# Kernel optimization log

Hardware: AMD Instinct MI355X
Metric: run time of the kernel (lower is better)

## Reference

```python
import jax, jax.numpy as jnp
import numpy as np

L, D, H, FFN, V = 24, 512, 16, 2048, 1025
HD = D // H
TOP_K = 15
REP_PEN = 1.35


def _layernorm(x, w, b, eps=1e-5):
    m = jnp.mean(x, -1, keepdims=True)
    var = jnp.var(x, -1, keepdims=True)
    return (x - m) / jnp.sqrt(var + eps) * w + b


def _sine_pe(T, d):
    pos = jnp.arange(T, dtype=jnp.float32)[:, None]
    div = jnp.exp(jnp.arange(0, d, 2, dtype=jnp.float32) * (-np.log(10000.0) / d))
    pe = jnp.zeros((T, d), jnp.float32)
    pe = pe.at[:, 0::2].set(jnp.sin(pos * div))
    pe = pe.at[:, 1::2].set(jnp.cos(pos * div))
    return pe


def setup_inputs():
    S, Ty, B = 2047, 1535, 1
    key = jax.random.key(0)
    ks = jax.random.split(key, 16)
    n = lambda i, sh, s=0.02: jax.random.normal(ks[i], sh, jnp.float32) * s
    return {
        "y": jax.random.randint(ks[0], (B, Ty + 1), 0, V, jnp.int32),
        "k": n(1, (L, S, B, D), 1.0),
        "v": n(2, (L, S, B, D), 1.0),
        "y_emb": n(3, (B, Ty, D), 1.0),
        "x_example": n(4, (B, 512), 1.0),
        "alpha": jnp.ones((1,), jnp.float32),
        "emb_table": n(5, (V, D)),
        "in_proj_w": n(6, (L, 3 * D, D)),
        "in_proj_b": jnp.zeros((L, 3 * D), jnp.float32),
        "out_w": n(7, (L, D, D)),
        "out_b": jnp.zeros((L, D), jnp.float32),
        "ln1_w": jnp.ones((L, D), jnp.float32),
        "ln1_b": jnp.zeros((L, D), jnp.float32),
        "ln2_w": jnp.ones((L, D), jnp.float32),
        "ln2_b": jnp.zeros((L, D), jnp.float32),
        "ffn_w1": n(8, (L, FFN, D)),
        "ffn_b1": jnp.zeros((L, FFN), jnp.float32),
        "ffn_w2": n(9, (L, D, FFN)),
        "ffn_b2": jnp.zeros((L, D), jnp.float32),
        "pred_w": n(10, (V, D)),
        "pred_b": jnp.zeros((V,), jnp.float32),
        "noise": jax.random.normal(ks[11], (V,), jnp.float32),
    }


def reference(y, k, v, y_emb, x_example, alpha, emb_table,
              in_proj_w, in_proj_b, out_w, out_b,
              ln1_w, ln1_b, ln2_w, ln2_b,
              ffn_w1, ffn_b1, ffn_w2, ffn_b2,
              pred_w, pred_b, noise):
    B = y.shape[0]
    # pad KV caches by one slot along seq dim (dim 1) -> [L, S+1, B, D]
    k_pad = jnp.pad(k, ((0, 0), (0, 1), (0, 0), (0, 0)))
    v_pad = jnp.pad(v, ((0, 0), (0, 1), (0, 0), (0, 0)))

    # embed newest token, extend y_emb cache
    new_emb = emb_table[y[:, -1:]]                       # [B,1,D]
    y_emb_new = jnp.concatenate([y_emb, new_emb], axis=1)  # [B,T,D]
    T = y_emb_new.shape[1]
    pe = _sine_pe(T, D)
    y_pos = y_emb_new + alpha * pe[None]                 # scale=False -> x_scale=1
    x = y_pos[:, -1:]                                    # [B,1,D] single query token

    scale = 1.0 / jnp.sqrt(jnp.float32(HD))

    def scan_body(x, per):
        kl, vl, wqkv, bqkv, wo, bo, g1, b1, g2, b2, fw1, fb1, fw2, fb2 = per
        qkv = jnp.einsum('bqd,ed->bqe', x, wqkv) + bqkv  # [B,1,3D]
        q, k_new, v_new = jnp.split(qkv, 3, axis=-1)
        kl = kl.at[-1].set(k_new[:, 0])                  # write into last cache slot
        vl = vl.at[-1].set(v_new[:, 0])
        qh = q.reshape(B, 1, H, HD)
        kh = kl.reshape(-1, B, H, HD)                    # [S+1,B,H,hd]
        vh = vl.reshape(-1, B, H, HD)
        scores = jnp.einsum('bqhd,sbhd->bhqs', qh, kh) * scale
        attn = jax.nn.softmax(scores, axis=-1)
        ctx = jnp.einsum('bhqs,sbhd->bqhd', attn, vh).reshape(B, 1, D)
        attn_out = jnp.einsum('bqd,ed->bqe', ctx, wo) + bo
        x = _layernorm(x + attn_out, g1, b1)             # post-LN (torch default)
        hdn = jax.nn.relu(jnp.einsum('bqd,fd->bqf', x, fw1) + fb1)
        ff = jnp.einsum('bqf,df->bqd', hdn, fw2) + fb2
        x = _layernorm(x + ff, g2, b2)
        return x, (kl, vl)

    x, (k_out, v_out) = jax.lax.scan(
        scan_body, x,
        (k_pad, v_pad, in_proj_w, in_proj_b, out_w, out_b,
         ln1_w, ln1_b, ln2_w, ln2_b, ffn_w1, ffn_b1, ffn_w2, ffn_b2))

    logits = jnp.einsum('bd,vd->bv', x[:, -1], pred_w) + pred_b  # [B,V]

    # ---- sampling on logits[0] ----
    lg = logits[0]
    prev = y[0]
    # repetition penalty (gather -> transform -> scatter; dup indices write same value)
    score = lg[prev]
    score = jnp.where(score < 0, score * REP_PEN, score / REP_PEN)
    lg = lg.at[prev].set(score)
    # top_p == 1.0 -> skipped; temperature == 1.0
    pivot = jax.lax.top_k(lg, TOP_K)[0][-1]
    lg = jnp.where(lg < pivot, -jnp.inf, lg)
    probs = jax.nn.softmax(lg)
    # faithful to source: argmax(probs / randn_like(probs))
    samples = jnp.argmax(probs / noise).astype(jnp.int32)[None, None]  # [1,1]
    y_new = jnp.concatenate([y, samples.astype(y.dtype)], axis=1)
    return y_new, k_out, v_out, y_emb_new, logits, samples
```

## Files before the change

### kernel.cpp

```cpp
#include <hip/hip_runtime.h>
#include <math.h>

#define LL 24
#define DD 512
#define HH 16
#define FFD 2048
#define VV 1025
#define SS 2047
#define TKV 2048
#define TYY 1535
#define NBLK 256
#define NT 512

typedef float f4v __attribute__((ext_vector_type(4)));

constexpr size_t O_YNEW  = 0;
constexpr size_t O_KOUT  = 1537;
constexpr size_t O_VOUT  = O_KOUT + (size_t)LL*TKV*DD;
constexpr size_t O_YEMB  = O_VOUT + (size_t)LL*TKV*DD;
constexpr size_t O_LOGITS= O_YEMB + (size_t)(TYY+1)*DD;
constexpr size_t O_SAMP  = O_LOGITS + VV;

constexpr int W_FFA  = 0;
constexpr int W_WY   = 8192;
constexpr int W_PART = 16384;
constexpr int W_KN   = 25088;
constexpr int W_VN   = 25600;

struct P {
  const int* y; const float* k; const float* v; const float* yemb;
  const float* alpha; const float* emb;
  const float* ipw; const float* ipb; const float* ow; const float* ob;
  const float* l1w; const float* l1b; const float* l2w; const float* l2b;
  const float* f1w; const float* f1b; const float* f2w; const float* f2b;
  const float* pw; const float* pb; const float* noise;
  float* out; float* ws;
};

__device__ __forceinline__ float dot4(float4 a, float4 b){
  return a.x*b.x + a.y*b.y + a.z*b.z + a.w*b.w;
}
__device__ __forceinline__ float ldv(const float* pp){
  return __hip_atomic_load(pp, __ATOMIC_RELAXED, __HIP_MEMORY_SCOPE_AGENT);
}
__device__ __forceinline__ void stv(float* pp, float v){
  __hip_atomic_store(pp, v, __ATOMIC_RELAXED, __HIP_MEMORY_SCOPE_AGENT);
}
__device__ __forceinline__ unsigned ldu(const unsigned* pp){
  return __hip_atomic_load(pp, __ATOMIC_RELAXED, __HIP_MEMORY_SCOPE_AGENT);
}

__device__ __forceinline__ void lbar(){
  asm volatile("s_waitcnt lgkmcnt(0)" ::: "memory");
  __builtin_amdgcn_s_barrier();
  __builtin_amdgcn_sched_barrier(0);
}
__device__ __forceinline__ void barr_arrive(unsigned* flags, unsigned ph){
  asm volatile("s_waitcnt vmcnt(0) lgkmcnt(0)" ::: "memory");
  __builtin_amdgcn_s_barrier();
  __builtin_amdgcn_sched_barrier(0);
  if (threadIdx.x == 0)
    __hip_atomic_store(&flags[blockIdx.x*16], ph, __ATOMIC_RELAXED, __HIP_MEMORY_SCOPE_AGENT);
}
__device__ __forceinline__ void barr_wait(unsigned* flags, unsigned ph){
  const int t = threadIdx.x;
  if (t < 64){
    for (;;){
      int ok = 1;
      #pragma unroll
      for (int i=0;i<4;++i) ok &= (int)(ldu(&flags[(t*4+i)*16]) >= ph);
      if (__all(ok)) break;
    }
  }
  __builtin_amdgcn_s_barrier();
  asm volatile("" ::: "memory");
}
__device__ __forceinline__ void barr_wait_head(unsigned* flags, unsigned ph, int h){
  const int t = threadIdx.x;
  if (t < 64){
    for (;;){
      int ok = 1;
      if (t < 16) ok = (int)(ldu(&flags[(t*16 + h)*16]) >= ph);
      if (__all(ok)) break;
    }
  }
  __builtin_amdgcn_s_barrier();
  asm volatile("" ::: "memory");
}

__device__ __forceinline__ float2 bsum2(float a, float b2, float2* r8, int t){
  for (int off=32; off; off>>=1){ a += __shfl_xor(a, off); b2 += __shfl_xor(b2, off); }
  lbar();
  if ((t & 63) == 0) r8[t >> 6] = make_float2(a, b2);
  lbar();
  float2 s = r8[0];
  #pragma unroll
  for (int i=1;i<8;++i){ s.x += r8[i].x; s.y += r8[i].y; }
  return s;
}
__device__ __forceinline__ void ln512g(float r, float g, float bb,
                                       float* dst, float2* r8, int t)
{
  float2 s = bsum2(r, r*r, r8, t);
  float mean = s.x * (1.f/512.f);
  float var  = fmaxf(s.y * (1.f/512.f) - mean*mean, 0.f);
  dst[t] = (r - mean) * rsqrtf(var + 1e-5f) * g + bb;
}
__device__ __forceinline__ void bargmax(float v, int i, float* r8v, int* r8i,
                                        int t, float& ov, int& oi)
{
  for (int off=32; off; off>>=1){
    float v2 = __shfl_xor(v, off); int i2 = __shfl_xor(i, off);
    if (v2 > v || (v2 == v && i2 < i)){ v = v2; i = i2; }
  }
  lbar();
  if ((t & 63) == 0){ r8v[t>>6] = v; r8i[t>>6] = i; }
  lbar();
  ov = r8v[0]; oi = r8i[0];
  #pragma unroll
  for (int kk=1; kk<8; ++kk){
    float v2 = r8v[kk]; int i2 = r8i[kk];
    if (v2 > ov || (v2 == ov && i2 < oi)){ ov = v2; oi = i2; }
  }
}

struct RegsQ  { float4 w[8]; float b[4]; };
struct RegsKV { float4 k0,k1,v0,v1; };
struct RegsTl { float4 t0,t1; float bias; };
struct RegsLN { float g2,b2,fb2; };
struct RegsBC { float2 oww; float4 f1p0,f1p1,f2p0,f2p1;
                float g1,b1,obv,f1bv; };

__device__ __forceinline__ void issueQ(const P& p, int l, int h, int t, RegsQ& q){
  const int lane = t & 63, w = t >> 6;
  const float* Wb = p.ipw + (size_t)l*1536*DD;
  const float* Bb = p.ipb + (size_t)l*1536;
  #pragma unroll
  for (int pp=0; pp<4; ++pp){
    int row = h*32 + w + 8*pp;
    const float4* wr = (const float4*)(Wb + (size_t)row*DD);
    q.w[2*pp] = wr[lane]; q.w[2*pp+1] = wr[lane+64];
    q.b[pp] = Bb[row];
  }
}
__device__ __forceinline__ void issueL(const P& p, int b, int t, RegsQ& q){
  const int lane = t & 63, w = t >> 6;
  int row = (w < 4) ? b*4 + w : ((b == 255 && w == 4) ? 1024 : -1);
  if (row >= 0){
    const float4* wr = (const float4*)(p.pw + (size_t)row*DD);
    q.w[0] = wr[lane]; q.w[1] = wr[lane+64];
    q.b[0] = p.pb[row];
  }
}
__device__ __forceinline__ void issueKV(const P& p, int l, int h, int c, int t,
                                        RegsKV& kv){
  const float* kb = p.k + (size_t)l*SS*DD;
  const float* vb = p.v + (size_t)l*SS*DD;
  const int s0 = c*128;
  kv.k0 = kv.v0 = kv.k1 = kv.v1 = make_float4(0,0,0,0);
  {
    int row = t >> 3, c4 = (t & 7)*4, s = s0 + row;
    if (s < SS){
      kv.k0 = *(const float4*)&kb[(size_t)s*DD + h*32 + c4];
      kv.v0 = *(const float4*)&vb[(size_t)s*DD + h*32 + c4];
    }
  }
  {
    int idx = t + NT;
    int row = idx >> 3, c4 = (idx & 7)*4, s = s0 + row;
    if (s < SS){
      kv.k1 = *(const float4*)&kb[(size_t)s*DD + h*32 + c4];
      kv.v1 = *(const float4*)&vb[(size_t)s*DD + h*32 + c4];
    }
  }
}
__device__ __forceinline__ void issueTl(const P& p, int l, int h, int c, int t,
                                        RegsTl& tl){
  const int lane = t & 63, w = t >> 6;
  if (w < 4){
    int isv = w >> 1;
    int row = 512 + isv*512 + h*32 + c*2 + (w&1);
    const float4* wr = (const float4*)(p.ipw + (size_t)l*1536*DD + (size_t)row*DD);
    tl.t0 = wr[lane]; tl.t1 = wr[lane+64];
    tl.bias = p.ipb[(size_t)l*1536 + row];
  }
}
__device__ __forceinline__ void issueLN(const P& p, int l, int t, RegsLN& r){
  r.g2 = p.l2w[(size_t)l*DD + t];
  r.b2 = p.l2b[(size_t)l*DD + t];
  r.fb2= p.f2b[(size_t)l*DD + t];
}
__device__ __forceinline__ void issueBCsmall(const P& p, int l, int b, int h,
                                             int c, int t, RegsBC& bc){
  bc.oww = *(const float2*)(p.ow + (size_t)l*DD*DD
            + (size_t)(c*32 + (t>>4))*DD + h*32 + (t&15)*2);
  bc.f1bv = p.f1b[(size_t)l*FFD + b*8 + (t>>6)];
  bc.g1  = p.l1w[(size_t)l*DD + t];
  bc.b1  = p.l1b[(size_t)l*DD + t];
  bc.obv = p.ob[(size_t)l*DD + t];
}
__device__ __forceinline__ void issueBCw(const P& p, int l, int b, int t,
                                         RegsBC& bc){
  const int lane = t & 63, w = t >> 6;
  {
    int f = b*8 + w;
    const float4* wr = (const float4*)(p.f1w + (size_t)l*FFD*DD + (size_t)f*DD);
    bc.f1p0 = wr[lane]; bc.f1p1 = wr[lane+64];
  }
  {
    const float* wr = p.f2w + (size_t)l*DD*FFD + (size_t)t*FFD + b*8;
    bc.f2p0 = *(const float4*)wr;
    bc.f2p1 = *(const float4*)(wr+4);
  }
}

__global__ __launch_bounds__(NT, 1) void mega_kernel(P p)
{
  __shared__ __align__(16) float S_kl[128*33];
  __shared__ __align__(16) float S_vl[128*33];
  __shared__ __align__(16) float S_x[512];
  __shared__ float S_ps[128];
  __shared__ float S_cacc[512];
  __shared__ float S_pb[544];
  __shared__ float S_q[32];
  __shared__ float S_kn[32];
  __shared__ float S_vn[32];
  __shared__ float S_ctx[32];
  __shared__ float S_scal[4];
  __shared__ float S_hdn[8];
  __shared__ float2 S_r82[8];
  __shared__ float S_r8v[8];
  __shared__ int   S_r8i[8];

  const int t = threadIdx.x, b = blockIdx.x;
  const int lane = t & 63, w = t >> 6;
  const int h = b & 15, c = b >> 4;
  unsigned* flags = (unsigned*)p.ws;
  float* wsd = p.ws + 4352;
  float* out = p.out;
  unsigned ph = 0;

  RegsQ q; RegsKV kv; RegsTl tl; RegsLN lnp; RegsBC bc;
  issueQ(p, 0, h, t, q);
  issueKV(p, 0, h, c, t, kv);
  issueTl(p, 0, h, c, t, tl);
  issueBCw(p, 0, b, t, bc);

  for (int l = 0; l < LL; ++l){
    float fs = 0.f;
    if (l > 0){
      const float* fb = wsd + W_FFA + (size_t)((l+1)&1)*4096;
      #pragma unroll
      for (int i=0;i<8;++i) fs += ldv(&fb[i*512 + t]);
    }
    issueBCsmall(p, l, b, h, c, t, bc);

    if (l == 0){
      int tok = p.y[1535];
      float a0 = p.alpha[0];
      float ev = p.emb[(size_t)tok*DD + t];
      float ang = 1535.0f * expf((float)(2*(t>>1)) * (-9.210340371976184f/512.0f));
      float pe = (t & 1) ? cosf(ang) : sinf(ang);
      S_x[t] = ev + a0*pe;
      if (b == 0) for (int i=t;i<1536;i+=NT)
        __builtin_nontemporal_store((float)p.y[i], out + O_YNEW + i);
      if (b == 1)
        __builtin_nontemporal_store(ev, out + O_YEMB + (size_t)TYY*DD + t);
      lbar();
    } else {
      float r = S_x[t] + lnp.fb2 + fs;
      ln512g(r, lnp.g2, lnp.b2, S_x, S_r82, t);
      lbar();
    }

    #pragma unroll
    for (int pp=0; pp<4; ++pp){
      float s = dot4(q.w[2*pp],   ((const float4*)S_x)[lane])
              + dot4(q.w[2*pp+1], ((const float4*)S_x)[lane+64]);
      for (int off=32; off; off>>=1) s += __shfl_xor(s, off);
      if (lane == 0) S_q[w + 8*pp] = s + q.b[pp];
    }
    if (w < 4){
      int isv = w >> 1;
      int col = h*32 + c*2 + (w & 1);
      float s = dot4(tl.t0, ((const float4*)S_x)[lane])
              + dot4(tl.t1, ((const float4*)S_x)[lane+64]);
      for (int off=32; off; off>>=1) s += __shfl_xor(s, off);
      if (lane == 0){
        float val = s + tl.bias;
        stv(&wsd[(isv ? W_VN : W_KN) + col], val);
        __builtin_nontemporal_store(val,
          out + (isv ? O_VOUT : O_KOUT) + (size_t)l*TKV*DD + (size_t)SS*DD + col);
      }
    }
    {
      int r0 = t >> 3, c40 = (t & 7)*4;
      int lb = r0*33 + c40;
      S_kl[lb+0]=kv.k0.x; S_kl[lb+1]=kv.k0.y; S_kl[lb+2]=kv.k0.z; S_kl[lb+3]=kv.k0.w;
      S_vl[lb+0]=kv.v0.x; S_vl[lb+1]=kv.v0.y; S_vl[lb+2]=kv.v0.z; S_vl[lb+3]=kv.v0.w;
      int idx = t + NT;
      int r1 = idx >> 3, c41 = (idx & 7)*4;
      int lb1 = r1*33 + c41;
      S_kl[lb1+0]=kv.k1.x; S_kl[lb1+1]=kv.k1.y; S_kl[lb1+2]=kv.k1.z; S_kl[lb1+3]=kv.k1.w;
      S_vl[lb1+0]=kv.v1.x; S_vl[lb1+1]=kv.v1.y; S_vl[lb1+2]=kv.v1.z; S_vl[lb1+3]=kv.v1.w;
    }
    lbar();

    {
      const int s0 = c*128;
      float pv = 0.f;
      if (t < 128 && (s0 + t) < SS){
        float acc = 0.f;
        #pragma unroll
        for (int j=0;j<32;++j) acc += S_kl[t*33+j]*S_q[j];
        pv = expf(acc * 0.17677669529663687f);
      }
      if (t < 128) S_ps[t] = pv;
      lbar();
      int g = t >> 5, j = t & 31;
      float ca = 0.f;
      #pragma unroll
      for (int i=0;i<8;++i){ int r = g*8+i; ca += S_ps[r]*S_vl[r*33+j]; }
      S_cacc[g*32 + j] = ca;
      lbar();
      float* pbase = wsd + W_PART + (size_t)(h*16+c)*34;
      if (t < 32){
        float v2 = 0.f;
        #pragma unroll
        for (int gg=0; gg<16; ++gg) v2 += S_cacc[gg*32 + t];
        stv(&pbase[t], v2);
      } else if (t >= 64 && t < 128){
        int ll2 = t - 64;
        float dv = S_ps[ll2] + S_ps[ll2+64];
        for (int off=32; off; off>>=1) dv += __shfl_xor(dv, off);
        if (ll2 == 0) stv(&pbase[32], dv);
      }
    }
    barr_arrive(flags, ++ph);
    {
      const int s0 = c*128;
      float* ko = out + O_KOUT + (size_t)l*TKV*DD;
      float* vo = out + O_VOUT + (size_t)l*TKV*DD;
      {
        int row = t >> 3, c4 = (t & 7)*4, s = s0 + row;
        if (s < SS){
          size_t go = (size_t)s*DD + h*32 + c4;
          __builtin_nontemporal_store(kv.k0.x, ko+go);
          __builtin_nontemporal_store(kv.k0.y, ko+go+1);
          __builtin_nontemporal_store(kv.k0.z, ko+go+2);
          __builtin_nontemporal_store(kv.k0.w, ko+go+3);
          __builtin_nontemporal_store(kv.v0.x, vo+go);
          __builtin_nontemporal_store(kv.v0.y, vo+go+1);
          __builtin_nontemporal_store(kv.v0.z, vo+go+2);
          __builtin_nontemporal_store(kv.v0.w, vo+go+3);
        }
      }
      {
        int idx = t + NT;
        int row = idx >> 3, c4 = (idx & 7)*4, s = s0 + row;
        if (s < SS){
          size_t go = (size_t)s*DD + h*32 + c4;
          __builtin_nontemporal_store(kv.k1.x, ko+go);
          __builtin_nontemporal_store(kv.k1.y, ko+go+1);
          __builtin_nontemporal_store(kv.k1.z, ko+go+2);
          __builtin_nontemporal_store(kv.k1.w, ko+go+3);
          __builtin_nontemporal_store(kv.v1.x, vo+go);
          __builtin_nontemporal_store(kv.v1.y, vo+go+1);
          __builtin_nontemporal_store(kv.v1.z, vo+go+2);
          __builtin_nontemporal_store(kv.v1.w, vo+go+3);
        }
      }
    }
    barr_wait_head(flags, ph, h);

    {
      for (int i=t; i<544; i+=NT) S_pb[i] = ldv(&wsd[W_PART + h*544 + i]);
      if (t < 32){ S_kn[t] = ldv(&wsd[W_KN + h*32 + t]); S_vn[t] = ldv(&wsd[W_VN + h*32 + t]); }
      lbar();
      if (t < 32){
        float tsp = S_q[t] * S_kn[t];
        for (int off=16; off; off>>=1) tsp += __shfl_xor(tsp, off, 32);
        if (t == 0){
          float et = expf(tsp * 0.17677669529663687f);
          float den = et;
          #pragma unroll
          for (int cc=0; cc<16; ++cc) den += S_pb[cc*34+32];
          S_scal[0] = et; S_scal[1] = den;
        }
      }
      lbar();
      if (t < 32){
        float cv = S_scal[0] * S_vn[t];
        #pragma unroll
        for (int cc=0; cc<16; ++cc) cv += S_pb[cc*34 + t];
        S_ctx[t] = cv / S_scal[1];
      }
      lbar();
      int j2 = (t & 15) * 2;
      float s = bc.oww.x*S_ctx[j2] + bc.oww.y*S_ctx[j2+1];
      s += __shfl_xor(s, 8, 16); s += __shfl_xor(s, 4, 16);
      s += __shfl_xor(s, 2, 16); s += __shfl_xor(s, 1, 16);
      if ((t & 15) == 0) stv(&wsd[W_WY + h*512 + c*32 + (t>>4)], s);
    }
    barr_arrive(flags, ++ph);
    if (l < 23){
      issueKV(p, l+1, h, c, t, kv);
      issueTl(p, l+1, h, c, t, tl);
    }
    issueLN(p, l, t, lnp);
    barr_wait(flags, ph);

    {
      float xs = 0.f;
      #pragma unroll
      for (int i=0;i<16;++i) xs += ldv(&wsd[W_WY + i*512 + t]);
      float r = S_x[t] + bc.obv + xs;
      ln512g(r, bc.g1, bc.b1, S_x, S_r82, t);
      lbar();
      {
        float s = dot4(bc.f1p0, ((const float4*)S_x)[lane])
                + dot4(bc.f1p1, ((const float4*)S_x)[lane+64]);
        for (int off=32; off; off>>=1) s += __shfl_xor(s, off);
        if (lane == 0) S_hdn[w] = fmaxf(s + bc.f1bv, 0.f);
      }
      lbar();
      float con = bc.f2p0.x*S_hdn[0]+bc.f2p0.y*S_hdn[1]
                + bc.f2p0.z*S_hdn[2]+bc.f2p0.w*S_hdn[3]
                + bc.f2p1.x*S_hdn[4]+bc.f2p1.y*S_hdn[5]
                + bc.f2p1.z*S_hdn[6]+bc.f2p1.w*S_hdn[7];
      atomicAdd(&wsd[W_FFA + (size_t)(l&1)*4096 + (size_t)(b&7)*512 + t], con);
      if (t < 16) stv(&wsd[W_FFA + (size_t)((l+1)&1)*4096 + b*16 + t], 0.f);
    }
    barr_arrive(flags, ++ph);
    if (l < 23){
      issueQ(p, l+1, h, t, q);
      issueBCw(p, l+1, b, t, bc);
    } else {
      issueL(p, b, t, q);
    }
    barr_wait(flags, ph);
  }

  {
    float fs = 0.f;
    const float* fb = wsd + W_FFA + (size_t)((LL-1)&1)*4096;
    #pragma unroll
    for (int i=0;i<8;++i) fs += ldv(&fb[i*512 + t]);
    float r = S_x[t] + lnp.fb2 + fs;
    ln512g(r, lnp.g2, lnp.b2, S_x, S_r82, t);
    lbar();
    if (w < 4 || (b == 255 && w == 4)){
      int row = (w < 4) ? b*4 + w : 1024;
      float s = dot4(q.w[0], ((const float4*)S_x)[lane])
              + dot4(q.w[1], ((const float4*)S_x)[lane+64]);
      for (int off=32; off; off>>=1) s += __shfl_xor(s, off);
      if (lane == 0) stv(&out[O_LOGITS+row], s + q.b[0]);
    }
  }
  barr_arrive(flags, ++ph);
  barr_wait(flags, ph);

  if (b == 0){
    float* lg  = S_kl;
    float* lgc = S_kl + 1025;
    int*   pen = (int*)(S_kl + 2050);
    for (int i=t;i<VV;i+=NT){ lg[i] = ldv(&out[O_LOGITS+i]); pen[i]=0; }
    lbar();
    for (int i=t;i<1536;i+=NT) pen[p.y[i]] = 1;
    lbar();
    for (int i=t;i<VV;i+=NT){
      if (pen[i]){ float s = lg[i]; lg[i] = (s<0.f) ? s*1.35f : s/1.35f; }
    }
    lbar();
    for (int i=t;i<VV;i+=NT) lgc[i]=lg[i];
    lbar();
    float sM = 0.f, sPiv = 0.f;
    for (int it=0; it<15; ++it){
      float bv = -INFINITY; int bi = VV;
      for (int i=t;i<VV;i+=NT){ float v2=lgc[i]; if (v2>bv){bv=v2;bi=i;} }
      float ov; int oi;
      bargmax(bv, bi, S_r8v, S_r8i, t, ov, oi);
      if (it==0)  sM   = ov;
      if (it==14) sPiv = ov;
      if (t==0) lgc[oi] = -INFINITY;
      lbar();
    }
    float zl = 0.f;
    for (int i=t;i<VV;i+=NT){
      float lv = lg[i];
      float pv2 = (lv < sPiv) ? 0.f : expf(lv - sM);
      lgc[i] = pv2; zl += pv2;
    }
    {
      float2 s = bsum2(zl, 0.f, S_r82, t);
      zl = s.x;
    }
    lbar();
    float bv=-INFINITY; int bi=VV;
    for (int i=t;i<VV;i+=NT){
      float val = (lgc[i]/zl)/p.noise[i];
      if (val>bv){bv=val;bi=i;}
    }
    float ov; int oi;
    bargmax(bv, bi, S_r8v, S_r8i, t, ov, oi);
    if (t==0){
      float sf = (float)oi;
      out[O_SAMP] = sf;
      out[O_YNEW+1536] = sf;
    }
  } else {
    const int nf4 = (TYY*DD - 4)/4;
    for (int qq = (b-1)*NT + t; qq < nf4; qq += 255*NT){
      float4 a = *(const float4*)&p.yemb[qq*4];
      float4 bq = *(const float4*)&p.yemb[qq*4 + 4];
      f4v o = {a.w, bq.x, bq.y, bq.z};
      __builtin_nontemporal_store(o, (f4v*)(out + O_YEMB + 3 + (size_t)qq*4));
    }
    if (b == 1){
      if (t < 3) __builtin_nontemporal_store(p.yemb[t], out + O_YEMB + t);
      if (t == 3) __builtin_nontemporal_store(p.yemb[TYY*DD-1], out + O_YEMB + TYY*DD - 1);
    }
  }
}

extern "C" void kernel_launch(void* const* d_in, const int* in_sizes, int n_in,
                              void* d_out, int out_size, void* d_ws, size_t ws_size,
                              hipStream_t stream)
{
  P p;
  p.y    = (const int*)d_in[0];
  p.k    = (const float*)d_in[1];
  p.v    = (const float*)d_in[2];
  p.yemb = (const float*)d_in[3];
  p.alpha= (const float*)d_in[5];
  p.emb  = (const float*)d_in[6];
  p.ipw  = (const float*)d_in[7];
  p.ipb  = (const float*)d_in[8];
  p.ow   = (const float*)d_in[9];
  p.ob   = (const float*)d_in[10];
  p.l1w  = (const float*)d_in[11];
  p.l1b  = (const float*)d_in[12];
  p.l2w  = (const float*)d_in[13];
  p.l2b  = (const float*)d_in[14];
  p.f1w  = (const float*)d_in[15];
  p.f1b  = (const float*)d_in[16];
  p.f2w  = (const float*)d_in[17];
  p.f2b  = (const float*)d_in[18];
  p.pw   = (const float*)d_in[19];
  p.pb   = (const float*)d_in[20];
  p.noise= (const float*)d_in[21];
  p.out  = (float*)d_out;
  p.ws   = (float*)d_ws;

  hipMemsetAsync(d_ws, 0, 50176, stream);
  void* args[] = { &p };
  hipLaunchCooperativeKernel((void*)mega_kernel, dim3(NBLK), dim3(NT), args, 0, stream);
}
```

Baseline: 470.7 us.

## Remove per-head barrier by atomically accumulating unnormalized attention output projections

Each block now multiplies its unnormalized partial attention numerator directly by its slice of the output projection and atomically adds the result into a double-buffered workspace. Softmax denominators are also atomically summed per head and applied as reciprocals when the residual is formed. This removes the per-head grid barrier phase and its partial-result gather. The chunk-15 block now computes the full new K/V rows for its head in place of the distributed per-block rows. The exchange is more atomic traffic, more registers for the larger Q/K/V weight prefetch, a larger workspace memset, and the new-token logit is no longer softmax-stabilized (it enters via exp through the shared path).

```diff
diff --git a/kernel.cpp b/kernel.cpp
--- a/kernel.cpp
+++ b/kernel.cpp
@@ -21,11 +21,9 @@
 constexpr size_t O_LOGITS= O_YEMB + (size_t)(TYY+1)*DD;
 constexpr size_t O_SAMP  = O_LOGITS + VV;
 
-constexpr int W_FFA  = 0;
-constexpr int W_WY   = 8192;
-constexpr int W_PART = 16384;
-constexpr int W_KN   = 25088;
-constexpr int W_VN   = 25600;
+constexpr int W_WYA = 0;
+constexpr int W_DEN = 16384;
+constexpr int W_FFA = 16896;
 
 struct P {
   const int* y; const float* k; const float* v; const float* yemb;
@@ -75,18 +73,6 @@
   __builtin_amdgcn_s_barrier();
   asm volatile("" ::: "memory");
 }
-__device__ __forceinline__ void barr_wait_head(unsigned* flags, unsigned ph, int h){
-  const int t = threadIdx.x;
-  if (t < 64){
-    for (;;){
-      int ok = 1;
-      if (t < 16) ok = (int)(ldu(&flags[(t*16 + h)*16]) >= ph);
-      if (__all(ok)) break;
-    }
-  }
-  __builtin_amdgcn_s_barrier();
-  asm volatile("" ::: "memory");
-}
 
 __device__ __forceinline__ float2 bsum2(float a, float b2, float2* r8, int t){
   for (int off=32; off; off>>=1){ a += __shfl_xor(a, off); b2 += __shfl_xor(b2, off); }
@@ -124,14 +110,14 @@
   }
 }
 
-struct RegsQ  { float4 w[8]; float b[4]; };
+struct RegsQX { float4 w[24]; float b[12]; };
 struct RegsKV { float4 k0,k1,v0,v1; };
-struct RegsTl { float4 t0,t1; float bias; };
 struct RegsLN { float g2,b2,fb2; };
-struct RegsBC { float2 oww; float4 f1p0,f1p1,f2p0,f2p1;
-                float g1,b1,obv,f1bv; };
-
-__device__ __forceinline__ void issueQ(const P& p, int l, int h, int t, RegsQ& q){
+struct RegsW  { float4 w[8]; };
+struct RegsBC { float4 f1p0,f1p1,f2p0,f2p1; float g1,b1,obv,f1bv; };
+
+__device__ __forceinline__ void issueQX(const P& p, int l, int h, int c, int t,
+                                        RegsQX& q){
   const int lane = t & 63, w = t >> 6;
   const float* Wb = p.ipw + (size_t)l*1536*DD;
   const float* Bb = p.ipb + (size_t)l*1536;
@@ -142,8 +128,18 @@
     q.w[2*pp] = wr[lane]; q.w[2*pp+1] = wr[lane+64];
     q.b[pp] = Bb[row];
   }
-}
-__device__ __forceinline__ void issueL(const P& p, int b, int t, RegsQ& q){
+  if (c == 15){
+    #pragma unroll
+    for (int pp=4; pp<12; ++pp){
+      int r = w + 8*((pp-4)&3);
+      int row = ((pp < 8) ? 512 : 1024) + h*32 + r;
+      const float4* wr = (const float4*)(Wb + (size_t)row*DD);
+      q.w[2*pp] = wr[lane]; q.w[2*pp+1] = wr[lane+64];
+      q.b[pp] = Bb[row];
+    }
+  }
+}
+__device__ __forceinline__ void issueL(const P& p, int b, int t, RegsQX& q){
   const int lane = t & 63, w = t >> 6;
   int row = (w < 4) ? b*4 + w : ((b == 255 && w == 4) ? 1024 : -1);
   if (row >= 0){
@@ -174,32 +170,24 @@
     }
   }
 }
-__device__ __forceinline__ void issueTl(const P& p, int l, int h, int c, int t,
-                                        RegsTl& tl){
-  const int lane = t & 63, w = t >> 6;
-  if (w < 4){
-    int isv = w >> 1;
-    int row = 512 + isv*512 + h*32 + c*2 + (w&1);
-    const float4* wr = (const float4*)(p.ipw + (size_t)l*1536*DD + (size_t)row*DD);
-    tl.t0 = wr[lane]; tl.t1 = wr[lane+64];
-    tl.bias = p.ipb[(size_t)l*1536 + row];
-  }
-}
 __device__ __forceinline__ void issueLN(const P& p, int l, int t, RegsLN& r){
   r.g2 = p.l2w[(size_t)l*DD + t];
   r.b2 = p.l2b[(size_t)l*DD + t];
   r.fb2= p.f2b[(size_t)l*DD + t];
 }
-__device__ __forceinline__ void issueBCsmall(const P& p, int l, int b, int h,
-                                             int c, int t, RegsBC& bc){
-  bc.oww = *(const float2*)(p.ow + (size_t)l*DD*DD
-            + (size_t)(c*32 + (t>>4))*DD + h*32 + (t&15)*2);
+__device__ __forceinline__ void issueW(const P& p, int l, int h, int t, RegsW& wsl){
+  const float4* wr = (const float4*)(p.ow + (size_t)l*DD*DD + (size_t)t*DD + h*32);
+  #pragma unroll
+  for (int i=0;i<8;++i) wsl.w[i] = wr[i];
+}
+__device__ __forceinline__ void issueBCsmall(const P& p, int l, int b, int t,
+                                             RegsBC& bc){
   bc.f1bv = p.f1b[(size_t)l*FFD + b*8 + (t>>6)];
   bc.g1  = p.l1w[(size_t)l*DD + t];
   bc.b1  = p.l1b[(size_t)l*DD + t];
   bc.obv = p.ob[(size_t)l*DD + t];
 }
-__device__ __forceinline__ void issueBCw(const P& p, int l, int b, int t,
+__device__ __forceinline__ void issueF12(const P& p, int l, int b, int t,
                                          RegsBC& bc){
   const int lane = t & 63, w = t >> 6;
   {
@@ -221,11 +209,9 @@
   __shared__ __align__(16) float S_x[512];
   __shared__ float S_ps[128];
   __shared__ float S_cacc[512];
-  __shared__ float S_pb[544];
   __shared__ float S_q[32];
-  __shared__ float S_kn[32];
-  __shared__ float S_vn[32];
-  __shared__ float S_ctx[32];
+  __shared__ __align__(16) float S_num[32];
+  __shared__ float S_rcp[16];
   __shared__ float S_scal[4];
   __shared__ float S_hdn[8];
   __shared__ float2 S_r82[8];
@@ -240,20 +226,20 @@
   float* out = p.out;
   unsigned ph = 0;
 
-  RegsQ q; RegsKV kv; RegsTl tl; RegsLN lnp; RegsBC bc;
-  issueQ(p, 0, h, t, q);
+  RegsQX qx; RegsKV kv; RegsLN lnp; RegsW wsl; RegsBC bc;
+  issueQX(p, 0, h, c, t, qx);
   issueKV(p, 0, h, c, t, kv);
-  issueTl(p, 0, h, c, t, tl);
-  issueBCw(p, 0, b, t, bc);
 
   for (int l = 0; l < LL; ++l){
+    const int par = l & 1, np = (l+1) & 1;
     float fs = 0.f;
     if (l > 0){
-      const float* fb = wsd + W_FFA + (size_t)((l+1)&1)*4096;
+      const float* fb = wsd + W_FFA + (size_t)np*4096;
       #pragma unroll
       for (int i=0;i<8;++i) fs += ldv(&fb[i*512 + t]);
     }
-    issueBCsmall(p, l, b, h, c, t, bc);
+    issueW(p, l, h, t, wsl);
+    issueBCsmall(p, l, b, t, bc);
 
     if (l == 0){
       int tok = p.y[1535];
@@ -275,41 +261,47 @@
 
     #pragma unroll
     for (int pp=0; pp<4; ++pp){
-      float s = dot4(q.w[2*pp],   ((const float4*)S_x)[lane])
-              + dot4(q.w[2*pp+1], ((const float4*)S_x)[lane+64]);
+      float s = dot4(qx.w[2*pp],   ((const float4*)S_x)[lane])
+              + dot4(qx.w[2*pp+1], ((const float4*)S_x)[lane+64]);
       for (int off=32; off; off>>=1) s += __shfl_xor(s, off);
-      if (lane == 0) S_q[w + 8*pp] = s + q.b[pp];
-    }
-    if (w < 4){
-      int isv = w >> 1;
-      int col = h*32 + c*2 + (w & 1);
-      float s = dot4(tl.t0, ((const float4*)S_x)[lane])
-              + dot4(tl.t1, ((const float4*)S_x)[lane+64]);
-      for (int off=32; off; off>>=1) s += __shfl_xor(s, off);
-      if (lane == 0){
-        float val = s + tl.bias;
-        stv(&wsd[(isv ? W_VN : W_KN) + col], val);
-        __builtin_nontemporal_store(val,
-          out + (isv ? O_VOUT : O_KOUT) + (size_t)l*TKV*DD + (size_t)SS*DD + col);
+      if (lane == 0) S_q[w + 8*pp] = s + qx.b[pp];
+    }
+    if (c == 15){
+      #pragma unroll
+      for (int pp=4; pp<12; ++pp){
+        float s = dot4(qx.w[2*pp],   ((const float4*)S_x)[lane])
+                + dot4(qx.w[2*pp+1], ((const float4*)S_x)[lane+64]);
+        for (int off=32; off; off>>=1) s += __shfl_xor(s, off);
+        if (lane == 0){
+          int r = w + 8*((pp-4)&3);
+          float val = s + qx.b[pp];
+          if (pp < 8) S_kl[127*33 + r] = val;
+          else        S_vl[127*33 + r] = val;
+          __builtin_nontemporal_store(val,
+            out + ((pp<8) ? O_KOUT : O_VOUT) + (size_t)l*TKV*DD + (size_t)SS*DD + h*32 + r);
+        }
       }
     }
     {
-      int r0 = t >> 3, c40 = (t & 7)*4;
-      int lb = r0*33 + c40;
-      S_kl[lb+0]=kv.k0.x; S_kl[lb+1]=kv.k0.y; S_kl[lb+2]=kv.k0.z; S_kl[lb+3]=kv.k0.w;
-      S_vl[lb+0]=kv.v0.x; S_vl[lb+1]=kv.v0.y; S_vl[lb+2]=kv.v0.z; S_vl[lb+3]=kv.v0.w;
+      int r0 = t >> 3, c40 = (t & 7)*4, s0c = c*128;
+      if (s0c + r0 < SS){
+        int lb = r0*33 + c40;
+        S_kl[lb+0]=kv.k0.x; S_kl[lb+1]=kv.k0.y; S_kl[lb+2]=kv.k0.z; S_kl[lb+3]=kv.k0.w;
+        S_vl[lb+0]=kv.v0.x; S_vl[lb+1]=kv.v0.y; S_vl[lb+2]=kv.v0.z; S_vl[lb+3]=kv.v0.w;
+      }
       int idx = t + NT;
       int r1 = idx >> 3, c41 = (idx & 7)*4;
-      int lb1 = r1*33 + c41;
-      S_kl[lb1+0]=kv.k1.x; S_kl[lb1+1]=kv.k1.y; S_kl[lb1+2]=kv.k1.z; S_kl[lb1+3]=kv.k1.w;
-      S_vl[lb1+0]=kv.v1.x; S_vl[lb1+1]=kv.v1.y; S_vl[lb1+2]=kv.v1.z; S_vl[lb1+3]=kv.v1.w;
+      if (s0c + r1 < SS){
+        int lb1 = r1*33 + c41;
+        S_kl[lb1+0]=kv.k1.x; S_kl[lb1+1]=kv.k1.y; S_kl[lb1+2]=kv.k1.z; S_kl[lb1+3]=kv.k1.w;
+        S_vl[lb1+0]=kv.v1.x; S_vl[lb1+1]=kv.v1.y; S_vl[lb1+2]=kv.v1.z; S_vl[lb1+3]=kv.v1.w;
+      }
     }
     lbar();
 
     {
-      const int s0 = c*128;
       float pv = 0.f;
-      if (t < 128 && (s0 + t) < SS){
+      if (t < 128){
         float acc = 0.f;
         #pragma unroll
         for (int j=0;j<32;++j) acc += S_kl[t*33+j]*S_q[j];
@@ -323,18 +315,22 @@
       for (int i=0;i<8;++i){ int r = g*8+i; ca += S_ps[r]*S_vl[r*33+j]; }
       S_cacc[g*32 + j] = ca;
       lbar();
-      float* pbase = wsd + W_PART + (size_t)(h*16+c)*34;
       if (t < 32){
         float v2 = 0.f;
         #pragma unroll
         for (int gg=0; gg<16; ++gg) v2 += S_cacc[gg*32 + t];
-        stv(&pbase[t], v2);
+        S_num[t] = v2;
       } else if (t >= 64 && t < 128){
         int ll2 = t - 64;
         float dv = S_ps[ll2] + S_ps[ll2+64];
         for (int off=32; off; off>>=1) dv += __shfl_xor(dv, off);
-        if (ll2 == 0) stv(&pbase[32], dv);
-      }
+        if (ll2 == 0) atomicAdd(&wsd[W_DEN + par*256 + h*16], dv);
+      }
+      lbar();
+      float yc = 0.f;
+      #pragma unroll
+      for (int i=0;i<8;++i) yc += dot4(wsl.w[i], ((const float4*)S_num)[i]);
+      atomicAdd(&wsd[W_WYA + par*8192 + h*512 + t], yc);
     }
     barr_arrive(flags, ++ph);
     {
@@ -371,49 +367,20 @@
         }
       }
     }
-    barr_wait_head(flags, ph, h);
-
-    {
-      for (int i=t; i<544; i+=NT) S_pb[i] = ldv(&wsd[W_PART + h*544 + i]);
-      if (t < 32){ S_kn[t] = ldv(&wsd[W_KN + h*32 + t]); S_vn[t] = ldv(&wsd[W_VN + h*32 + t]); }
-      lbar();
-      if (t < 32){
-        float tsp = S_q[t] * S_kn[t];
-        for (int off=16; off; off>>=1) tsp += __shfl_xor(tsp, off, 32);
-        if (t == 0){
-          float et = expf(tsp * 0.17677669529663687f);
-          float den = et;
-          #pragma unroll
-          for (int cc=0; cc<16; ++cc) den += S_pb[cc*34+32];
-          S_scal[0] = et; S_scal[1] = den;
-        }
-      }
-      lbar();
-      if (t < 32){
-        float cv = S_scal[0] * S_vn[t];
-        #pragma unroll
-        for (int cc=0; cc<16; ++cc) cv += S_pb[cc*34 + t];
-        S_ctx[t] = cv / S_scal[1];
-      }
-      lbar();
-      int j2 = (t & 15) * 2;
-      float s = bc.oww.x*S_ctx[j2] + bc.oww.y*S_ctx[j2+1];
-      s += __shfl_xor(s, 8, 16); s += __shfl_xor(s, 4, 16);
-      s += __shfl_xor(s, 2, 16); s += __shfl_xor(s, 1, 16);
-      if ((t & 15) == 0) stv(&wsd[W_WY + h*512 + c*32 + (t>>4)], s);
-    }
-    barr_arrive(flags, ++ph);
-    if (l < 23){
-      issueKV(p, l+1, h, c, t, kv);
-      issueTl(p, l+1, h, c, t, tl);
-    }
+    issueF12(p, l, b, t, bc);
     issueLN(p, l, t, lnp);
     barr_wait(flags, ph);
 
     {
+      float wv[16];
+      #pragma unroll
+      for (int hh=0; hh<16; ++hh)
+        wv[hh] = ldv(&wsd[W_WYA + par*8192 + hh*512 + t]);
+      if (t < 16) S_rcp[t] = 1.f / ldv(&wsd[W_DEN + par*256 + t*16]);
+      lbar();
       float xs = 0.f;
       #pragma unroll
-      for (int i=0;i<16;++i) xs += ldv(&wsd[W_WY + i*512 + t]);
+      for (int hh=0; hh<16; ++hh) xs += wv[hh] * S_rcp[hh];
       float r = S_x[t] + bc.obv + xs;
       ln512g(r, bc.g1, bc.b1, S_x, S_r82, t);
       lbar();
@@ -428,15 +395,17 @@
                 + bc.f2p0.z*S_hdn[2]+bc.f2p0.w*S_hdn[3]
                 + bc.f2p1.x*S_hdn[4]+bc.f2p1.y*S_hdn[5]
                 + bc.f2p1.z*S_hdn[6]+bc.f2p1.w*S_hdn[7];
-      atomicAdd(&wsd[W_FFA + (size_t)(l&1)*4096 + (size_t)(b&7)*512 + t], con);
-      if (t < 16) stv(&wsd[W_FFA + (size_t)((l+1)&1)*4096 + b*16 + t], 0.f);
+      atomicAdd(&wsd[W_FFA + (size_t)par*4096 + (size_t)(b&7)*512 + t], con);
+      if (t < 16) stv(&wsd[W_FFA + (size_t)np*4096 + b*16 + t], 0.f);
+      if (t < 32) stv(&wsd[W_WYA + (size_t)np*8192 + b*32 + t], 0.f);
+      if (b < 16 && t == 0) stv(&wsd[W_DEN + np*256 + b*16], 0.f);
     }
     barr_arrive(flags, ++ph);
     if (l < 23){
-      issueQ(p, l+1, h, t, q);
-      issueBCw(p, l+1, b, t, bc);
+      issueQX(p, l+1, h, c, t, qx);
+      issueKV(p, l+1, h, c, t, kv);
     } else {
-      issueL(p, b, t, q);
+      issueL(p, b, t, qx);
     }
     barr_wait(flags, ph);
   }
@@ -451,10 +420,10 @@
     lbar();
     if (w < 4 || (b == 255 && w == 4)){
       int row = (w < 4) ? b*4 + w : 1024;
-      float s = dot4(q.w[0], ((const float4*)S_x)[lane])
-              + dot4(q.w[1], ((const float4*)S_x)[lane+64]);
+      float s = dot4(qx.w[0], ((const float4*)S_x)[lane])
+              + dot4(qx.w[1], ((const float4*)S_x)[lane+64]);
       for (int off=32; off; off>>=1) s += __shfl_xor(s, off);
-      if (lane == 0) stv(&out[O_LOGITS+row], s + q.b[0]);
+      if (lane == 0) stv(&out[O_LOGITS+row], s + qx.b[0]);
     }
   }
   barr_arrive(flags, ++ph);
@@ -552,7 +521,7 @@
   p.out  = (float*)d_out;
   p.ws   = (float*)d_ws;
 
-  hipMemsetAsync(d_ws, 0, 50176, stream);
+  hipMemsetAsync(d_ws, 0, 117760, stream);
   void* args[] = { &p };
   hipLaunchCooperativeKernel((void*)mega_kernel, dim3(NBLK), dim3(NT), args, 0, stream);
 }
```

Result: slower. 902.2 us (+91.7%).
